# Optimization experiments

Measured on AMD Instinct MI355X. Metric: run time of the kernel, lower is better.

Reference implementation:

```python
import jax, jax.numpy as jnp
import numpy as np

N = 10000      # nodes per node type
E = 80000      # edges per relation
IN = 64        # input feature dim per node type
H = 128        # hidden_channels per layer
OUT = 64       # final out_channels
R = 12         # relations: all ordered pairs of 4 node types
# node-type order: 0=state, 1=action, 2=background, 3=t
# relation order follows: for k1 in types: for k2 in types: if k1!=k2
SRC_T = jnp.array([0,0,0,1,1,1,2,2,2,3,3,3], dtype=jnp.int32)
DST_T = jnp.array([1,2,3,0,2,3,0,1,3,0,1,2], dtype=jnp.int32)


def setup_inputs() -> dict:
    key = jax.random.key(0)
    ks = jax.random.split(key, 20)
    inp = {
        'x_state':      jax.random.normal(ks[0], (N, IN), jnp.float32),
        'x_action':     jax.random.normal(ks[1], (N, IN), jnp.float32),
        'x_background': jax.random.normal(ks[2], (N, IN), jnp.float32),
        'x_t':          jax.random.normal(ks[3], (N, IN), jnp.float32),
        'edge_index':   jax.random.randint(ks[4], (R, 2, E), 0, N, jnp.int32),
        # layer 0 GAT params (stacked over 12 relations)
        'Wsrc0': jax.random.normal(ks[5], (R, IN, H), jnp.float32) * 0.05,
        'Wdst0': jax.random.normal(ks[6], (R, IN, H), jnp.float32) * 0.05,
        'asrc0': jax.random.normal(ks[7], (R, H), jnp.float32) * 0.05,
        'adst0': jax.random.normal(ks[8], (R, H), jnp.float32) * 0.05,
        'b0':    jnp.zeros((R, H), jnp.float32),
        # layer 1
        'Wsrc1': jax.random.normal(ks[9], (R, H, H), jnp.float32) * 0.05,
        'Wdst1': jax.random.normal(ks[10], (R, H, H), jnp.float32) * 0.05,
        'asrc1': jax.random.normal(ks[11], (R, H), jnp.float32) * 0.05,
        'adst1': jax.random.normal(ks[12], (R, H), jnp.float32) * 0.05,
        'b1':    jnp.zeros((R, H), jnp.float32),
        # final linear on 'state'
        'lin_w': jax.random.normal(ks[13], (H, OUT), jnp.float32) * 0.05,
        'lin_b': jnp.zeros((OUT,), jnp.float32),
    }
    return inp


def _gat(X, ei, Wsrc, Wdst, asrc, adst, bias, s_t, d_t):
    # X: [4, N, D] stacked node features; one GATConv relation (heads=1)
    n = X.shape[1]
    xs = X[s_t] @ Wsrc                      # [N, H] transformed src feats
    xd = X[d_t] @ Wdst                      # [N, H]
    src, dst = ei[0], ei[1]                 # [E]
    a_s = xs @ asrc                         # [N] (x_src * att_src).sum(-1)
    a_d = xd @ adst                         # [N]
    e = jax.nn.leaky_relu(a_s[src] + a_d[dst], 0.2)    # [E]
    # softmax over incoming edges per destination node
    m = jax.ops.segment_max(e, dst, num_segments=n)
    w = jnp.exp(e - m[dst])
    den = jax.ops.segment_sum(w, dst, num_segments=n)
    alpha = w / den[dst]                    # [E]
    msg = alpha[:, None] * xs[src]          # [E, H]
    out = jax.ops.segment_sum(msg, dst, num_segments=n)
    return out + bias                       # [N, H]


def _layer(X, ei, Wsrc, Wdst, asrc, adst, bias):
    out_r = jax.vmap(_gat, in_axes=(None, 0, 0, 0, 0, 0, 0, 0, 0))(
        X, ei, Wsrc, Wdst, asrc, adst, bias, SRC_T, DST_T)   # [R, N, H]
    # HeteroConv aggr='sum': sum relation outputs into their dst node types
    out = jnp.zeros((4, X.shape[1], Wsrc.shape[-1]), out_r.dtype).at[DST_T].add(out_r)
    return jax.nn.relu(out)


def reference(x_state, x_action, x_background, x_t, edge_index,
              Wsrc0, Wdst0, asrc0, adst0, b0,
              Wsrc1, Wdst1, asrc1, adst1, b1,
              lin_w, lin_b):
    X = jnp.stack([x_state, x_action, x_background, x_t])   # [4, N, IN]
    X = _layer(X, edge_index, Wsrc0, Wdst0, asrc0, adst0, b0)
    X = _layer(X, edge_index, Wsrc1, Wdst1, asrc1, adst1, b1)
    return X[0] @ lin_w + lin_b             # Linear on x_dict['state']
```

## Files before the change

### kernel.cpp

```cpp
#include <hip/hip_runtime.h>
#include <cfloat>
#include <cmath>

#define N_NODES 10000
#define E_EDGES 80000
#define R_REL   12
#define H_DIM   128
#define IN_DIM  64
#define OUT_DIM 64

__global__ void hist_kernel(const int* __restrict__ EI, int* __restrict__ cnt) {
  int e = blockIdx.x * blockDim.x + threadIdx.x;
  int r = blockIdx.y;
  if (e >= E_EDGES) return;
  int dst = EI[(2 * r + 1) * E_EDGES + e];
  atomicAdd(&cnt[r * N_NODES + dst], 1);
}

#define SCAN_E 10
__global__ __launch_bounds__(1024) void scan_kernel(int* __restrict__ cnt,
                                                    int* __restrict__ off) {
  const int r = blockIdx.x;
  const int t = threadIdx.x;
  const int lane = t & 63, wv = t >> 6;
  __shared__ int wsum[16];

  const int base = t * SCAN_E;
  int v[SCAN_E];
  int s = 0;
  #pragma unroll
  for (int k = 0; k < SCAN_E; ++k) {
    int i = base + k;
    v[k] = (i < N_NODES) ? cnt[r * N_NODES + i] : 0;
    s += v[k];
  }
  int incl = s;
  #pragma unroll
  for (int o = 1; o < 64; o <<= 1) {
    int u = __shfl_up(incl, o);
    if (lane >= o) incl += u;
  }
  if (lane == 63) wsum[wv] = incl;
  __syncthreads();
  if (wv == 0) {
    int ws = (lane < 16) ? wsum[lane] : 0;
    int wi = ws;
    #pragma unroll
    for (int o = 1; o < 16; o <<= 1) {
      int u = __shfl_up(wi, o);
      if (lane >= o) wi += u;
    }
    if (lane < 16) wsum[lane] = wi - ws;
  }
  __syncthreads();
  int run = wsum[wv] + incl - s;
  #pragma unroll
  for (int k = 0; k < SCAN_E; ++k) {
    int i = base + k;
    if (i < N_NODES) {
      off[r * (N_NODES + 1) + i] = run;
      cnt[r * N_NODES + i] = run;
      run += v[k];
    }
  }
  if (t == 1023) off[r * (N_NODES + 1) + N_NODES] = run;
}

__global__ void fill_kernel(const int* __restrict__ EI, int* __restrict__ cur,
                            int* __restrict__ EL) {
  int e = blockIdx.x * blockDim.x + threadIdx.x;
  int r = blockIdx.y;
  if (e >= E_EDGES) return;
  int dst = EI[(2 * r + 1) * E_EDGES + e];
  int src = EI[(2 * r + 0) * E_EDGES + e];
  int pos = atomicAdd(&cur[r * N_NODES + dst], 1);
  EL[r * E_EDGES + pos] = src;
}

template <int K>
__global__ void vcomp_kernel(const float* __restrict__ Wsrc, const float* __restrict__ asrc,
                             const float* __restrict__ Wdst, const float* __restrict__ adst,
                             float* __restrict__ VS, float* __restrict__ VD) {
  const int r = blockIdx.x;
  const int k = threadIdx.x;
  const float* w1 = Wsrc + ((size_t)r * K + k) * H_DIM;
  const float* w2 = Wdst + ((size_t)r * K + k) * H_DIM;
  const float* a1 = asrc + r * H_DIM;
  const float* a2 = adst + r * H_DIM;
  float s1 = 0.f, s2 = 0.f;
  for (int h = 0; h < H_DIM; ++h) {
    s1 = fmaf(w1[h], a1[h], s1);
    s2 = fmaf(w2[h], a2[h], s2);
  }
  VS[r * H_DIM + k] = s1;
  VD[r * H_DIM + k] = s2;
}

template <int K, bool PRUNED>
__global__ __launch_bounds__(256) void gemm_xs_kernel(
    const float* __restrict__ p0, const float* __restrict__ p1,
    const float* __restrict__ p2, const float* __restrict__ p3,
    const float* __restrict__ W,
    float* __restrict__ XS) {
  const int r = PRUNED ? 3 * (blockIdx.y + 1) : blockIdx.y;
  const int s = PRUNED ? (blockIdx.y + 1) : (r / 3);
  const float* __restrict__ X = (s == 0) ? p0 : (s == 1) ? p1 : (s == 2) ? p2 : p3;
  const int row0 = blockIdx.x * 128;
  const int tid = threadIdx.x;
  const int tx = tid & 15, ty = tid >> 4;
  __shared__ float Xst[32][132];
  __shared__ float Ws[32][132];

  float acc[8][8];
  #pragma unroll
  for (int i = 0; i < 8; ++i)
    #pragma unroll
    for (int j = 0; j < 8; ++j) acc[i][j] = 0.f;

  const float* Wr = W + (size_t)r * K * H_DIM;

  #pragma unroll 1
  for (int k0 = 0; k0 < K; k0 += 32) {
    #pragma unroll
    for (int p = 0; p < 4; ++p) {
      int idx = tid + p * 256;
      int row = idx >> 3;
      int kq = idx & 7;
      float4 v = {0.f, 0.f, 0.f, 0.f};
      int grow = row0 + row;
      if (grow < N_NODES)
        v = *(const float4*)(X + (size_t)grow * K + k0 + kq * 4);
      Xst[kq * 4 + 0][row] = v.x;
      Xst[kq * 4 + 1][row] = v.y;
      Xst[kq * 4 + 2][row] = v.z;
      Xst[kq * 4 + 3][row] = v.w;
    }
    #pragma unroll
    for (int p = 0; p < 4; ++p) {
      int idx = tid + p * 256;
      int kk = idx >> 5;
      int cq = idx & 31;
      float4 v = *(const float4*)(Wr + (size_t)(k0 + kk) * H_DIM + cq * 4);
      *(float4*)&Ws[kk][cq * 4] = v;
    }
    __syncthreads();
    #pragma unroll
    for (int kk = 0; kk < 32; ++kk) {
      float a[8], b[8];
      *(float4*)&a[0] = *(float4*)&Xst[kk][ty * 8];
      *(float4*)&a[4] = *(float4*)&Xst[kk][ty * 8 + 4];
      *(float4*)&b[0] = *(float4*)&Ws[kk][tx * 8];
      *(float4*)&b[4] = *(float4*)&Ws[kk][tx * 8 + 4];
      #pragma unroll
      for (int i = 0; i < 8; ++i)
        #pragma unroll
        for (int j = 0; j < 8; ++j) acc[i][j] = fmaf(a[i], b[j], acc[i][j]);
    }
    __syncthreads();
  }
  float* outp = XS + (size_t)r * N_NODES * H_DIM;
  #pragma unroll
  for (int i = 0; i < 8; ++i) {
    int row = row0 + ty * 8 + i;
    if (row < N_NODES) {
      *(float4*)(outp + (size_t)row * H_DIM + tx * 8) = *(float4*)&acc[i][0];
      *(float4*)(outp + (size_t)row * H_DIM + tx * 8 + 4) = *(float4*)&acc[i][4];
    }
  }
}

template <int K, bool PRUNED>
__global__ __launch_bounds__(256) void attn_coef_kernel(
    const float* __restrict__ p0, const float* __restrict__ p1,
    const float* __restrict__ p2, const float* __restrict__ p3,
    const float* __restrict__ VS, const float* __restrict__ VD,
    float* __restrict__ AS, float* __restrict__ AD) {
  const int nrel = PRUNED ? 3 : R_REL;
  const int lane = threadIdx.x & 63;
  const int wv = (blockIdx.x << 2) + (threadIdx.x >> 6);
  if (wv >= nrel * N_NODES) return;
  const int rr = wv / N_NODES;
  const int n = wv - rr * N_NODES;
  const int r = PRUNED ? 3 * (rr + 1) : rr;
  const int s = PRUNED ? (rr + 1) : (r / 3);
  int d;
  if (PRUNED) {
    d = 0;
  } else {
    const int j = r - s * 3;
    d = (j < s) ? j : j + 1;
  }
  const float* Xs = (s == 0) ? p0 : (s == 1) ? p1 : (s == 2) ? p2 : p3;
  const float* Xd = (d == 0) ? p0 : (d == 1) ? p1 : (d == 2) ? p2 : p3;
  float a_s, a_d;
  if (K == 128) {
    a_s = Xs[(size_t)n * K + lane] * VS[r * H_DIM + lane]
        + Xs[(size_t)n * K + 64 + lane] * VS[r * H_DIM + 64 + lane];
    a_d = Xd[(size_t)n * K + lane] * VD[r * H_DIM + lane]
        + Xd[(size_t)n * K + 64 + lane] * VD[r * H_DIM + 64 + lane];
  } else {
    a_s = Xs[(size_t)n * K + lane] * VS[r * H_DIM + lane];
    a_d = Xd[(size_t)n * K + lane] * VD[r * H_DIM + lane];
  }
  #pragma unroll
  for (int o = 32; o; o >>= 1) {
    a_s += __shfl_xor(a_s, o);
    a_d += __shfl_xor(a_d, o);
  }
  if (lane == 0) {
    AS[r * N_NODES + n] = a_s;
    AD[r * N_NODES + n] = a_d;
  }
}

template <bool PRUNED>
__global__ void edge_as_kernel(const float* __restrict__ AS, const int* __restrict__ EL,
                               float* __restrict__ ASE) {
  int i = blockIdx.x * blockDim.x + threadIdx.x;
  int r = PRUNED ? 3 * (blockIdx.y + 1) : blockIdx.y;
  if (i >= E_EDGES) return;
  ASE[r * E_EDGES + i] = AS[r * N_NODES + EL[r * E_EDGES + i]];
}

__global__ __launch_bounds__(256) void gather_kernel(
    const float* __restrict__ XS, const float* __restrict__ ASE,
    const float* __restrict__ AD, const int* __restrict__ off,
    const int* __restrict__ EL, const float* __restrict__ bias,
    float* __restrict__ Xout) {
  const int lane = threadIdx.x & 63;
  const int node = (blockIdx.x << 2) + (threadIdx.x >> 6);
  const int t = blockIdx.y;
  float acc0 = 0.f, acc1 = 0.f;
  #pragma unroll
  for (int j2 = 0; j2 < 3; ++j2) {
    const int s = (j2 < t) ? j2 : j2 + 1;
    const int r = s * 3 + ((t < s) ? t : t - 1);
    acc0 += bias[r * H_DIM + lane];
    acc1 += bias[r * H_DIM + 64 + lane];
    const int beg = off[r * (N_NODES + 1) + node];
    const int end = off[r * (N_NODES + 1) + node + 1];
    if (beg == end) continue;
    const float ad = AD[r * N_NODES + node];
    const float* aseR = ASE + (size_t)r * E_EDGES;
    const int* elR = EL + (size_t)r * E_EDGES;
    const float* xsR = XS + (size_t)r * N_NODES * H_DIM;
    float m = -FLT_MAX;
    for (int base = beg; base < end; base += 64) {
      int i = base + lane;
      float e = -FLT_MAX;
      if (i < end) {
        e = aseR[i] + ad;
        e = (e > 0.f) ? e : 0.2f * e;
      }
      #pragma unroll
      for (int o = 32; o; o >>= 1) e = fmaxf(e, __shfl_xor(e, o));
      m = fmaxf(m, e);
    }
    float den = 0.f, a0 = 0.f, a1 = 0.f;
    for (int base = beg; base < end; base += 64) {
      int i = base + lane;
      int nv = min(64, end - base);
      float w = 0.f;
      int src = 0;
      if (i < end) {
        src = elR[i];
        float e = aseR[i] + ad;
        e = (e > 0.f) ? e : 0.2f * e;
        w = exp2f(1.44269504f * (e - m));
      }
      float ws = w;
      #pragma unroll
      for (int o = 32; o; o >>= 1) ws += __shfl_xor(ws, o);
      den += ws;
      int j = 0;
      for (; j + 1 < nv; j += 2) {
        float wj0 = __shfl(w, j);
        float wj1 = __shfl(w, j + 1);
        int sj0 = __shfl(src, j);
        int sj1 = __shfl(src, j + 1);
        const float* row0 = xsR + (size_t)sj0 * H_DIM;
        const float* row1 = xsR + (size_t)sj1 * H_DIM;
        float x00 = row0[lane];
        float x01 = row0[64 + lane];
        float x10 = row1[lane];
        float x11 = row1[64 + lane];
        a0 = fmaf(wj0, x00, a0);
        a1 = fmaf(wj0, x01, a1);
        a0 = fmaf(wj1, x10, a0);
        a1 = fmaf(wj1, x11, a1);
      }
      if (j < nv) {
        float wj = __shfl(w, j);
        int sj = __shfl(src, j);
        const float* row = xsR + (size_t)sj * H_DIM;
        a0 = fmaf(wj, row[lane], a0);
        a1 = fmaf(wj, row[64 + lane], a1);
      }
    }
    float inv = 1.f / den;
    acc0 = fmaf(a0, inv, acc0);
    acc1 = fmaf(a1, inv, acc1);
  }
  acc0 = fmaxf(acc0, 0.f);
  acc1 = fmaxf(acc1, 0.f);
  float* o = Xout + ((size_t)t * N_NODES + node) * H_DIM;
  o[lane] = acc0;
  o[64 + lane] = acc1;
}

__global__ __launch_bounds__(256) void final_kernel(
    const float* __restrict__ X, const float* __restrict__ LW,
    const float* __restrict__ LB, float* __restrict__ out) {
  const int lane = threadIdx.x & 63;
  const int node = (blockIdx.x << 2) + (threadIdx.x >> 6);
  float xlo = X[(size_t)node * H_DIM + lane];
  float xhi = X[(size_t)node * H_DIM + 64 + lane];
  float acc = LB[lane];
  #pragma unroll
  for (int k = 0; k < 64; ++k) acc = fmaf(__shfl(xlo, k), LW[k * OUT_DIM + lane], acc);
  #pragma unroll
  for (int k = 0; k < 64; ++k) acc = fmaf(__shfl(xhi, k), LW[(64 + k) * OUT_DIM + lane], acc);
  out[(size_t)node * OUT_DIM + lane] = acc;
}

extern "C" void kernel_launch(void* const* d_in, const int* in_sizes, int n_in,
                              void* d_out, int out_size, void* d_ws, size_t ws_size,
                              hipStream_t stream) {
  (void)in_sizes; (void)n_in; (void)out_size; (void)ws_size;
  const float* x_state = (const float*)d_in[0];
  const float* x_action = (const float*)d_in[1];
  const float* x_bg = (const float*)d_in[2];
  const float* x_tt = (const float*)d_in[3];
  const int* EI = (const int*)d_in[4];
  const float* Wsrc0 = (const float*)d_in[5];
  const float* Wdst0 = (const float*)d_in[6];
  const float* asrc0 = (const float*)d_in[7];
  const float* adst0 = (const float*)d_in[8];
  const float* b0 = (const float*)d_in[9];
  const float* Wsrc1 = (const float*)d_in[10];
  const float* Wdst1 = (const float*)d_in[11];
  const float* asrc1 = (const float*)d_in[12];
  const float* adst1 = (const float*)d_in[13];
  const float* b1 = (const float*)d_in[14];
  const float* lin_w = (const float*)d_in[15];
  const float* lin_b = (const float*)d_in[16];
  float* out = (float*)d_out;

  char* p = (char*)d_ws;
  auto carve = [&](size_t bytes) -> void* {
    void* q = (void*)p;
    p += (bytes + 255) & ~(size_t)255;
    return q;
  };
  float* XS = (float*)carve(sizeof(float) * (size_t)R_REL * N_NODES * H_DIM);
  float* Xa = (float*)carve(sizeof(float) * (size_t)4 * N_NODES * H_DIM);
  float* Xb = (float*)carve(sizeof(float) * (size_t)N_NODES * H_DIM);
  float* AS = (float*)carve(sizeof(float) * (size_t)R_REL * N_NODES);
  float* AD = (float*)carve(sizeof(float) * (size_t)R_REL * N_NODES);
  float* ASE = (float*)carve(sizeof(float) * (size_t)R_REL * E_EDGES);
  float* VS = (float*)carve(sizeof(float) * (size_t)R_REL * H_DIM);
  float* VD = (float*)carve(sizeof(float) * (size_t)R_REL * H_DIM);
  int* CNT = (int*)carve(sizeof(int) * (size_t)R_REL * N_NODES);
  int* OFF = (int*)carve(sizeof(int) * (size_t)R_REL * (N_NODES + 1));
  int* EL = (int*)carve(sizeof(int) * (size_t)R_REL * E_EDGES);

  hipMemsetAsync(CNT, 0, sizeof(int) * (size_t)R_REL * N_NODES, stream);
  dim3 ge((E_EDGES + 255) / 256, R_REL);
  hist_kernel<<<ge, 256, 0, stream>>>(EI, CNT);
  scan_kernel<<<R_REL, 1024, 0, stream>>>(CNT, OFF);
  fill_kernel<<<ge, 256, 0, stream>>>(EI, CNT, EL);

  vcomp_kernel<IN_DIM><<<R_REL, IN_DIM, 0, stream>>>(Wsrc0, asrc0, Wdst0, adst0, VS, VD);
  gemm_xs_kernel<IN_DIM, false><<<dim3((N_NODES + 127) / 128, R_REL), 256, 0, stream>>>(
      x_state, x_action, x_bg, x_tt, Wsrc0, XS);
  attn_coef_kernel<IN_DIM, false><<<(R_REL * N_NODES) / 4, 256, 0, stream>>>(
      x_state, x_action, x_bg, x_tt, VS, VD, AS, AD);
  edge_as_kernel<false><<<dim3((E_EDGES + 255) / 256, R_REL), 256, 0, stream>>>(AS, EL, ASE);
  gather_kernel<<<dim3(N_NODES / 4, 4), 256, 0, stream>>>(XS, ASE, AD, OFF, EL, b0, Xa);

  const float* a0p = Xa;
  const float* a1p = Xa + (size_t)N_NODES * H_DIM;
  const float* a2p = Xa + (size_t)2 * N_NODES * H_DIM;
  const float* a3p = Xa + (size_t)3 * N_NODES * H_DIM;
  vcomp_kernel<H_DIM><<<R_REL, H_DIM, 0, stream>>>(Wsrc1, asrc1, Wdst1, adst1, VS, VD);
  gemm_xs_kernel<H_DIM, true><<<dim3((N_NODES + 127) / 128, 3), 256, 0, stream>>>(
      a0p, a1p, a2p, a3p, Wsrc1, XS);
  attn_coef_kernel<H_DIM, true><<<(3 * N_NODES) / 4, 256, 0, stream>>>(
      a0p, a1p, a2p, a3p, VS, VD, AS, AD);
  edge_as_kernel<true><<<dim3((E_EDGES + 255) / 256, 3), 256, 0, stream>>>(AS, EL, ASE);
  gather_kernel<<<dim3(N_NODES / 4, 1), 256, 0, stream>>>(XS, ASE, AD, OFF, EL, b1, Xb);

  final_kernel<<<N_NODES / 4, 256, 0, stream>>>(Xb, lin_w, lin_b, out);
}
```

Measured before the change: 401.9 us.

## Precompute unnormalized edge softmax weights and drop max pass in gather

```diff
diff --git a/kernel.cpp b/kernel.cpp
--- a/kernel.cpp
+++ b/kernel.cpp
@@ -67,7 +67,7 @@
 }
 
 __global__ void fill_kernel(const int* __restrict__ EI, int* __restrict__ cur,
-                            int* __restrict__ EL) {
+                            int* __restrict__ EL, int* __restrict__ DL) {
   int e = blockIdx.x * blockDim.x + threadIdx.x;
   int r = blockIdx.y;
   if (e >= E_EDGES) return;
@@ -75,6 +75,7 @@
   int src = EI[(2 * r + 0) * E_EDGES + e];
   int pos = atomicAdd(&cur[r * N_NODES + dst], 1);
   EL[r * E_EDGES + pos] = src;
+  DL[r * E_EDGES + pos] = dst;
 }
 
 template <int K>
@@ -214,19 +215,21 @@
 }
 
 template <bool PRUNED>
-__global__ void edge_as_kernel(const float* __restrict__ AS, const int* __restrict__ EL,
-                               float* __restrict__ ASE) {
+__global__ void edge_w_kernel(const float* __restrict__ AS, const float* __restrict__ AD,
+                              const int* __restrict__ EL, const int* __restrict__ DL,
+                              float* __restrict__ WE) {
   int i = blockIdx.x * blockDim.x + threadIdx.x;
   int r = PRUNED ? 3 * (blockIdx.y + 1) : blockIdx.y;
   if (i >= E_EDGES) return;
-  ASE[r * E_EDGES + i] = AS[r * N_NODES + EL[r * E_EDGES + i]];
+  float e = AS[r * N_NODES + EL[r * E_EDGES + i]] + AD[r * N_NODES + DL[r * E_EDGES + i]];
+  e = (e > 0.f) ? e : 0.2f * e;
+  WE[r * E_EDGES + i] = exp2f(1.44269504f * e);
 }
 
 __global__ __launch_bounds__(256) void gather_kernel(
-    const float* __restrict__ XS, const float* __restrict__ ASE,
-    const float* __restrict__ AD, const int* __restrict__ off,
-    const int* __restrict__ EL, const float* __restrict__ bias,
-    float* __restrict__ Xout) {
+    const float* __restrict__ XS, const float* __restrict__ WE,
+    const int* __restrict__ off, const int* __restrict__ EL,
+    const float* __restrict__ bias, float* __restrict__ Xout) {
   const int lane = threadIdx.x & 63;
   const int node = (blockIdx.x << 2) + (threadIdx.x >> 6);
   const int t = blockIdx.y;
@@ -235,66 +238,48 @@
   for (int j2 = 0; j2 < 3; ++j2) {
     const int s = (j2 < t) ? j2 : j2 + 1;
     const int r = s * 3 + ((t < s) ? t : t - 1);
-    acc0 += bias[r * H_DIM + lane];
-    acc1 += bias[r * H_DIM + 64 + lane];
+    float2 bv = *(const float2*)(bias + r * H_DIM + 2 * lane);
+    acc0 += bv.x;
+    acc1 += bv.y;
     const int beg = off[r * (N_NODES + 1) + node];
     const int end = off[r * (N_NODES + 1) + node + 1];
     if (beg == end) continue;
-    const float ad = AD[r * N_NODES + node];
-    const float* aseR = ASE + (size_t)r * E_EDGES;
+    const float* weR = WE + (size_t)r * E_EDGES;
     const int* elR = EL + (size_t)r * E_EDGES;
     const float* xsR = XS + (size_t)r * N_NODES * H_DIM;
-    float m = -FLT_MAX;
-    for (int base = beg; base < end; base += 64) {
-      int i = base + lane;
-      float e = -FLT_MAX;
-      if (i < end) {
-        e = aseR[i] + ad;
-        e = (e > 0.f) ? e : 0.2f * e;
-      }
-      #pragma unroll
-      for (int o = 32; o; o >>= 1) e = fmaxf(e, __shfl_xor(e, o));
-      m = fmaxf(m, e);
-    }
     float den = 0.f, a0 = 0.f, a1 = 0.f;
     for (int base = beg; base < end; base += 64) {
       int i = base + lane;
-      int nv = min(64, end - base);
       float w = 0.f;
       int src = 0;
       if (i < end) {
+        w = weR[i];
         src = elR[i];
-        float e = aseR[i] + ad;
-        e = (e > 0.f) ? e : 0.2f * e;
-        w = exp2f(1.44269504f * (e - m));
       }
       float ws = w;
       #pragma unroll
       for (int o = 32; o; o >>= 1) ws += __shfl_xor(ws, o);
       den += ws;
+      int nv = min(64, end - base);
       int j = 0;
       for (; j + 1 < nv; j += 2) {
         float wj0 = __shfl(w, j);
         float wj1 = __shfl(w, j + 1);
         int sj0 = __shfl(src, j);
         int sj1 = __shfl(src, j + 1);
-        const float* row0 = xsR + (size_t)sj0 * H_DIM;
-        const float* row1 = xsR + (size_t)sj1 * H_DIM;
-        float x00 = row0[lane];
-        float x01 = row0[64 + lane];
-        float x10 = row1[lane];
-        float x11 = row1[64 + lane];
-        a0 = fmaf(wj0, x00, a0);
-        a1 = fmaf(wj0, x01, a1);
-        a0 = fmaf(wj1, x10, a0);
-        a1 = fmaf(wj1, x11, a1);
+        float2 x0 = *(const float2*)(xsR + (size_t)sj0 * H_DIM + 2 * lane);
+        float2 x1 = *(const float2*)(xsR + (size_t)sj1 * H_DIM + 2 * lane);
+        a0 = fmaf(wj0, x0.x, a0);
+        a1 = fmaf(wj0, x0.y, a1);
+        a0 = fmaf(wj1, x1.x, a0);
+        a1 = fmaf(wj1, x1.y, a1);
       }
       if (j < nv) {
         float wj = __shfl(w, j);
         int sj = __shfl(src, j);
-        const float* row = xsR + (size_t)sj * H_DIM;
-        a0 = fmaf(wj, row[lane], a0);
-        a1 = fmaf(wj, row[64 + lane], a1);
+        float2 x0 = *(const float2*)(xsR + (size_t)sj * H_DIM + 2 * lane);
+        a0 = fmaf(wj, x0.x, a0);
+        a1 = fmaf(wj, x0.y, a1);
       }
     }
     float inv = 1.f / den;
@@ -303,9 +288,8 @@
   }
   acc0 = fmaxf(acc0, 0.f);
   acc1 = fmaxf(acc1, 0.f);
-  float* o = Xout + ((size_t)t * N_NODES + node) * H_DIM;
-  o[lane] = acc0;
-  o[64 + lane] = acc1;
+  float2 ov = {acc0, acc1};
+  *(float2*)(Xout + ((size_t)t * N_NODES + node) * H_DIM + 2 * lane) = ov;
 }
 
 __global__ __launch_bounds__(256) void final_kernel(
@@ -357,26 +341,28 @@
   float* Xb = (float*)carve(sizeof(float) * (size_t)N_NODES * H_DIM);
   float* AS = (float*)carve(sizeof(float) * (size_t)R_REL * N_NODES);
   float* AD = (float*)carve(sizeof(float) * (size_t)R_REL * N_NODES);
-  float* ASE = (float*)carve(sizeof(float) * (size_t)R_REL * E_EDGES);
+  float* WE = (float*)carve(sizeof(float) * (size_t)R_REL * E_EDGES);
   float* VS = (float*)carve(sizeof(float) * (size_t)R_REL * H_DIM);
   float* VD = (float*)carve(sizeof(float) * (size_t)R_REL * H_DIM);
   int* CNT = (int*)carve(sizeof(int) * (size_t)R_REL * N_NODES);
   int* OFF = (int*)carve(sizeof(int) * (size_t)R_REL * (N_NODES + 1));
   int* EL = (int*)carve(sizeof(int) * (size_t)R_REL * E_EDGES);
+  int* DL = (int*)carve(sizeof(int) * (size_t)R_REL * E_EDGES);
 
   hipMemsetAsync(CNT, 0, sizeof(int) * (size_t)R_REL * N_NODES, stream);
   dim3 ge((E_EDGES + 255) / 256, R_REL);
   hist_kernel<<<ge, 256, 0, stream>>>(EI, CNT);
   scan_kernel<<<R_REL, 1024, 0, stream>>>(CNT, OFF);
-  fill_kernel<<<ge, 256, 0, stream>>>(EI, CNT, EL);
+  fill_kernel<<<ge, 256, 0, stream>>>(EI, CNT, EL, DL);
 
   vcomp_kernel<IN_DIM><<<R_REL, IN_DIM, 0, stream>>>(Wsrc0, asrc0, Wdst0, adst0, VS, VD);
   gemm_xs_kernel<IN_DIM, false><<<dim3((N_NODES + 127) / 128, R_REL), 256, 0, stream>>>(
       x_state, x_action, x_bg, x_tt, Wsrc0, XS);
   attn_coef_kernel<IN_DIM, false><<<(R_REL * N_NODES) / 4, 256, 0, stream>>>(
       x_state, x_action, x_bg, x_tt, VS, VD, AS, AD);
-  edge_as_kernel<false><<<dim3((E_EDGES + 255) / 256, R_REL), 256, 0, stream>>>(AS, EL, ASE);
-  gather_kernel<<<dim3(N_NODES / 4, 4), 256, 0, stream>>>(XS, ASE, AD, OFF, EL, b0, Xa);
+  edge_w_kernel<false><<<dim3((E_EDGES + 255) / 256, R_REL), 256, 0, stream>>>(
+      AS, AD, EL, DL, WE);
+  gather_kernel<<<dim3(N_NODES / 4, 4), 256, 0, stream>>>(XS, WE, OFF, EL, b0, Xa);
 
   const float* a0p = Xa;
   const float* a1p = Xa + (size_t)N_NODES * H_DIM;
@@ -387,8 +373,9 @@
       a0p, a1p, a2p, a3p, Wsrc1, XS);
   attn_coef_kernel<H_DIM, true><<<(3 * N_NODES) / 4, 256, 0, stream>>>(
       a0p, a1p, a2p, a3p, VS, VD, AS, AD);
-  edge_as_kernel<true><<<dim3((E_EDGES + 255) / 256, 3), 256, 0, stream>>>(AS, EL, ASE);
-  gather_kernel<<<dim3(N_NODES / 4, 1), 256, 0, stream>>>(XS, ASE, AD, OFF, EL, b1, Xb);
+  edge_w_kernel<true><<<dim3((E_EDGES + 255) / 256, 3), 256, 0, stream>>>(
+      AS, AD, EL, DL, WE);
+  gather_kernel<<<dim3(N_NODES / 4, 1), 256, 0, stream>>>(XS, WE, OFF, EL, b1, Xb);
 
   final_kernel<<<N_NODES / 4, 256, 0, stream>>>(Xb, lin_w, lin_b, out);
 }
```

After: 408.2 us. Within noise of the previous version (+1.6%).
